# Optimization experiments

Hardware: AMD Instinct MI355X
Metric: run time of the kernel (lower is better)

## Reference

```python
import jax, jax.numpy as jnp
import numpy as np

GRID_SPACING = 0.5  # tf.constant(0.5)


def _mlp(x, W1, b1, W2, b2, W3, b3):
    # tiny base_model: 3 -> H -> H -> 1, positive output (softplus head)
    h = jnp.tanh(x @ W1 + b1)
    h = jnp.tanh(h @ W2 + b2)
    return jax.nn.softplus(h @ W3 + b3)


def setup_inputs() -> dict:
    key = jax.random.key(0)
    ks = jax.random.split(key, 8)
    nx = ny = nz = 128
    N = nx * ny * nz
    Ns = (nx - 1) * (ny - 1) * (nz - 1)
    B, H = 32768, 128
    DATAX = jax.random.uniform(ks[0], (N, 3), dtype=jnp.float32)
    DATAF = jax.random.uniform(ks[1], (N, 1), dtype=jnp.float32)
    STAGX = jax.random.uniform(ks[2], (Ns, 3), dtype=jnp.float32)
    LAPLF = jax.random.uniform(ks[3], (nx - 2, ny - 2, nz - 2), dtype=jnp.float32)
    center_indices = jax.random.randint(ks[4], (B,), 0, N, dtype=jnp.int32)
    W1 = jax.random.normal(ks[5], (3, H), dtype=jnp.float32) * 0.5
    W2 = jax.random.normal(ks[6], (H, H), dtype=jnp.float32) * (1.0 / np.sqrt(H))
    W3 = jax.random.normal(ks[7], (H, 1), dtype=jnp.float32) * (1.0 / np.sqrt(H))
    return {
        'DATAX': DATAX, 'DATAF': DATAF, 'STAGX': STAGX, 'LAPLF': LAPLF,
        'loss_m_weight': jnp.full((1,), 0.5, dtype=jnp.float32),
        'W1': W1, 'b1': jnp.zeros((H,), jnp.float32),
        'W2': W2, 'b2': jnp.zeros((H,), jnp.float32),
        'W3': W3, 'b3': jnp.zeros((1,), jnp.float32),
        'center_indices': center_indices,
    }


def reference(DATAX, DATAF, STAGX, LAPLF, loss_m_weight,
              W1, b1, W2, b2, W3, b3, center_indices):
    nxm2, nym2, nzm2 = LAPLF.shape
    nx, ny, nz = nxm2 + 2, nym2 + 2, nzm2 + 2
    N = nx * ny * nz
    Ns = (nx - 1) * (ny - 1) * (nz - 1)
    ci = center_indices.astype(jnp.int32)

    # decode flat id (z-major: z*nx*ny + y*nx + x)
    i_z = ci // (nx * ny)
    rem = ci % (nx * ny)
    i_y = rem // nx
    i_x = rem % nx
    valid = ((i_x >= 1) & (i_x < nx - 1) & (i_y >= 1) & (i_y < ny - 1)
             & (i_z >= 1) & (i_z < nz - 1))

    # 8 original-grid corners: dx,dy,dz in {-1,1}, dz fastest (list-comp order)
    off = jnp.array([-1, 1], jnp.int32)
    dd = jnp.stack(jnp.meshgrid(off, off, off, indexing='ij'), -1).reshape(8, 3)
    ox = i_x[:, None] + dd[None, :, 0]
    oy = i_y[:, None] + dd[None, :, 1]
    oz = i_z[:, None] + dd[None, :, 2]
    flat_o = jnp.clip(oz * nx * ny + oy * nx + ox, 0, N - 1)  # [B,8]

    # 8 staggered-grid corners: dx,dy,dz in {-1,0}, flat = x*ny'*nz' + y*nz' + z
    offs = jnp.array([-1, 0], jnp.int32)
    ds = jnp.stack(jnp.meshgrid(offs, offs, offs, indexing='ij'), -1).reshape(8, 3)
    sx = i_x[:, None] + ds[None, :, 0]
    sy = i_y[:, None] + ds[None, :, 1]
    sz = i_z[:, None] + ds[None, :, 2]
    flat_s = jnp.clip(sx * (ny - 1) * (nz - 1) + sy * (nz - 1) + sz, 0, Ns - 1)

    fo = _mlp(DATAX[flat_o], W1, b1, W2, b2, W3, b3)[..., 0]  # [B,8]
    fs = _mlp(STAGX[flat_s], W1, b1, W2, b2, W3, b3)[..., 0]  # [B,8]

    # diagonals of the [2,2,2] cube: (000,111),(010,101),(001,110),(011,100)
    ia = jnp.array([0, 2, 1, 3])
    ib = jnp.array([7, 5, 6, 4])
    num = jnp.abs(fo[:, ia] + fo[:, ib] - fs[:, ia] - fs[:, ib])
    den = fo[:, ia] + fo[:, ib] + fs[:, ia] + fs[:, ib]
    delta = 3.0 * (GRID_SPACING ** 2)
    lap = jnp.sum(num / den, axis=1) / (3.0 * delta)  # [B]

    flat_l = jnp.clip((i_x - 1) * nym2 * nzm2 + (i_y - 1) * nzm2 + (i_z - 1),
                      0, nxm2 * nym2 * nzm2 - 1)
    dlap = LAPLF.reshape(-1)[flat_l] - lap
    m = valid.astype(dlap.dtype)
    loss_m = loss_m_weight[0] * (jnp.sum(jnp.square(dlap) * m)
                                 / jnp.maximum(jnp.sum(m), 1.0))

    pred = _mlp(DATAX[ci], W1, b1, W2, b2, W3, b3)[:, 0]
    loss_e = jnp.mean(jnp.abs(pred - DATAF[ci][:, 0]))
    return loss_e + loss_m
```

## Files before the change

### kernel.cpp

```cpp
#include <hip/hip_runtime.h>
#include <stdint.h>

#define NXC   128
#define NXY   16384
#define NTOT  2097152
#define NS    2048383
#define SXY   16129
#define SYC   127
#define LXY   15876
#define LTOT  2000376

#define SCALE 2.8853900817779268f

typedef __bf16 bf16x8 __attribute__((ext_vector_type(8)));
typedef float f32x4 __attribute__((ext_vector_type(4)));

typedef const __attribute__((address_space(1))) uint32_t* gas_t;
typedef __attribute__((address_space(3))) uint32_t* las_t;

__device__ __forceinline__ float rcp_hw(float x) {
#if __has_builtin(__builtin_amdgcn_rcpf)
  return __builtin_amdgcn_rcpf(x);
#else
  return 1.0f / x;
#endif
}
__device__ __forceinline__ float exp2_hw(float x) {
#if __has_builtin(__builtin_amdgcn_exp2f)
  return __builtin_amdgcn_exp2f(x);
#else
  return __exp2f(x);
#endif
}

__device__ __forceinline__ float tanh_pre(float z) {
  float e = exp2_hw(z);
  return fmaf(-2.0f, rcp_hw(e + 1.0f), 1.0f);
}

__device__ __forceinline__ float softplus_f(float x) {
  float a = fabsf(x);
  return fmaxf(x, 0.0f) + __logf(1.0f + __expf(-a));
}

__device__ __forceinline__ void ld8(const float* p, float* o) {
  float4 a = *reinterpret_cast<const float4*>(p);
  float4 b = *reinterpret_cast<const float4*>(p + 4);
  o[0] = a.x; o[1] = a.y; o[2] = a.z; o[3] = a.w;
  o[4] = b.x; o[5] = b.y; o[6] = b.z; o[7] = b.w;
}

__global__ __launch_bounds__(256) void conv_kernel(
    const float* __restrict__ W1, const float* __restrict__ B1,
    const float* __restrict__ W2, const float* __restrict__ B2,
    const float* __restrict__ W3,
    __bf16* __restrict__ w2pre, float* __restrict__ smallpre)
{
  const int n = blockIdx.x * 256 + threadIdx.x;
  if (n < 2048) {
    const int c = n >> 7, j = n & 127;
    bf16x8 v;
    #pragma unroll
    for (int e = 0; e < 8; ++e) v[e] = (__bf16)(SCALE * W2[(8 * c + e) * 128 + j]);
    *reinterpret_cast<bf16x8*>(&w2pre[(j << 7) + (((c ^ (j & 15)) & 15) << 3)]) = v;
  }
  if (blockIdx.x == 0) {
    for (int i = threadIdx.x; i < 768; i += 256) {
      float v;
      if (i < 384)      v = SCALE * W1[i];
      else if (i < 512) v = SCALE * B1[i - 384];
      else if (i < 640) v = SCALE * B2[i - 512];
      else              v = W3[i - 640];
      smallpre[i] = v;
    }
  }
}

__global__ __launch_bounds__(512) void mlp_kernel(
    const float* __restrict__ DATAX, const float* __restrict__ STAGX,
    const int* __restrict__ CI,
    const __bf16* __restrict__ w2pre, const float* __restrict__ smallpre,
    const float* __restrict__ B3, float* __restrict__ fout)
{
  __shared__ __align__(16) __bf16 w2t[16384];
  __shared__ __align__(16) float smallb[768];

  const int tid  = threadIdx.x;
  const int lane = tid & 63;
  const int wid  = tid >> 6;
  const int cl   = lane & 15;
  const int g    = lane >> 4;

  const int group = (blockIdx.x << 3) + wid;
  const int gbase = group << 6;
  const int p = gbase + lane;
  const unsigned bb = (unsigned)p / 17u;
  const int t = p - (int)bb * 17;
  const int ci = CI[bb];

  {
    const char* gsrc = (const char*)w2pre + (wid << 12) + (lane << 4);
    char*       ldst = (char*)w2t + (wid << 12);
    #pragma unroll
    for (int i = 0; i < 4; ++i) {
      __builtin_amdgcn_global_load_lds(
          (gas_t)(const void*)(gsrc + (i << 10)),
          (las_t)(void*)(ldst + (i << 10)), 16, 0, 0);
    }
    if (wid == 7) {
      const char* gs = (const char*)smallpre + (lane << 4);
      char*       ld = (char*)smallb;
      #pragma unroll
      for (int i = 0; i < 3; ++i) {
        __builtin_amdgcn_global_load_lds(
            (gas_t)(const void*)(gs + (i << 10)),
            (las_t)(void*)(ld + (i << 10)), 16, 0, 0);
      }
    }
  }

  const int iz = ci >> 14, rem = ci & 16383, iy = rem >> 7, ix = rem & 127;
  const float* xp;
  if (t < 8) {
    int ox = ix + ((t & 4) ? 1 : -1);
    int oy = iy + ((t & 2) ? 1 : -1);
    int oz = iz + ((t & 1) ? 1 : -1);
    int fl = oz * NXY + oy * NXC + ox;
    fl = min(max(fl, 0), NTOT - 1);
    xp = DATAX + 3 * fl;
  } else if (t < 16) {
    int ts = t - 8;
    int sx = ix + ((ts & 4) ? 0 : -1);
    int sy = iy + ((ts & 2) ? 0 : -1);
    int sz = iz + ((ts & 1) ? 0 : -1);
    int fl = sx * SXY + sy * SYC + sz;
    fl = min(max(fl, 0), NS - 1);
    xp = STAGX + 3 * fl;
  } else {
    xp = DATAX + 3 * ci;
  }
  const float px = xp[0], py = xp[1], pz = xp[2];
  const float b3v = B3[0];

  __syncthreads();

  const float* w1s = smallb;
  const float* b1s = smallb + 384;
  const float* b2s = smallb + 512;
  const float* w3s = smallb + 640;

  float rxv[4], ryv[4], rzv[4];
  #pragma unroll
  for (int mt = 0; mt < 4; ++mt) {
    int src = (mt << 4) + cl;
    rxv[mt] = __shfl(px, src);
    ryv[mt] = __shfl(py, src);
    rzv[mt] = __shfl(pz, src);
  }

  bf16x8 A[4][4];
  #pragma unroll
  for (int kt = 0; kt < 4; ++kt) {
    int k0 = (kt << 5) + (g << 3);
    float wx[8], wy[8], wz[8], bv[8];
    ld8(&w1s[k0], wx);
    ld8(&w1s[128 + k0], wy);
    ld8(&w1s[256 + k0], wz);
    ld8(&b1s[k0], bv);
    #pragma unroll
    for (int mt = 0; mt < 4; ++mt) {
      #pragma unroll
      for (int e = 0; e < 8; ++e) {
        float pre = fmaf(rxv[mt], wx[e],
                    fmaf(ryv[mt], wy[e],
                    fmaf(rzv[mt], wz[e], bv[e])));
        A[mt][kt][e] = (__bf16)tanh_pre(pre);
      }
    }
  }

  float s[4][4];
  #pragma unroll
  for (int mt = 0; mt < 4; ++mt)
    #pragma unroll
    for (int r = 0; r < 4; ++r) s[mt][r] = 0.f;

  #pragma unroll
  for (int nt = 0; nt < 8; ++nt) {
    const float b2v = b2s[cl + (nt << 4)];
    const float w3v = w3s[cl + (nt << 4)];
    f32x4 cc[4];
    #pragma unroll
    for (int mt = 0; mt < 4; ++mt) {
      f32x4 seed = {b2v, b2v, b2v, b2v};
      cc[mt] = seed;
    }
    const int row = (nt << 4) + cl;
    #pragma unroll
    for (int kt = 0; kt < 4; ++kt) {
      int chunk = (kt << 2) + g;
      bf16x8 bfv = *reinterpret_cast<const bf16x8*>(
          &w2t[(row << 7) + ((chunk ^ cl) << 3)]);
      #pragma unroll
      for (int mt = 0; mt < 4; ++mt)
        cc[mt] = __builtin_amdgcn_mfma_f32_16x16x32_bf16(A[mt][kt], bfv, cc[mt], 0, 0, 0);
    }
    #pragma unroll
    for (int mt = 0; mt < 4; ++mt) {
      #pragma unroll
      for (int r = 0; r < 4; ++r) {
        float h2 = tanh_pre(cc[mt][r]);
        s[mt][r] = fmaf(h2, w3v, s[mt][r]);
      }
    }
  }

  #pragma unroll
  for (int mt = 0; mt < 4; ++mt) {
    #pragma unroll
    for (int r = 0; r < 4; ++r) {
      float v = s[mt][r];
      v += __shfl_xor(v, 1);
      v += __shfl_xor(v, 2);
      v += __shfl_xor(v, 4);
      v += __shfl_xor(v, 8);
      s[mt][r] = v;
    }
  }
  if (cl == 0) {
    #pragma unroll
    for (int mt = 0; mt < 4; ++mt) {
      int base = gbase + (mt << 4) + (g << 2);
      float4 o;
      o.x = softplus_f(s[mt][0] + b3v);
      o.y = softplus_f(s[mt][1] + b3v);
      o.z = softplus_f(s[mt][2] + b3v);
      o.w = softplus_f(s[mt][3] + b3v);
      *reinterpret_cast<float4*>(&fout[base]) = o;
    }
  }
}

__global__ __launch_bounds__(256) void reduce1(
    const float* __restrict__ f, const int* __restrict__ CI,
    const float* __restrict__ LAPLF, const float* __restrict__ DATAF,
    float* __restrict__ partials, int B)
{
  const int tid = threadIdx.x;
  const int b = blockIdx.x * 256 + tid;
  float sq = 0.f, mv = 0.f, ae = 0.f;
  if (b < B) {
    int ci = CI[b];
    int iz = ci >> 14, rem = ci & 16383, iy = rem >> 7, ix = rem & 127;
    bool valid = (ix >= 1) & (ix < 127) & (iy >= 1) & (iy < 127) &
                 (iz >= 1) & (iz < 127);
    const float* fb = f + b * 17;
    float fo[8], fs[8];
    #pragma unroll
    for (int i = 0; i < 8; ++i) { fo[i] = fb[i]; fs[i] = fb[8 + i]; }
    float pred = fb[16];
    const int ia[4] = {0, 2, 1, 3};
    const int ib[4] = {7, 5, 6, 4};
    float lap = 0.f;
    #pragma unroll
    for (int r = 0; r < 4; ++r) {
      float aa = fo[ia[r]] + fo[ib[r]];
      float bs = fs[ia[r]] + fs[ib[r]];
      lap += fabsf(aa - bs) / (aa + bs);
    }
    lap *= (1.0f / 2.25f);
    int fl = (ix - 1) * LXY + (iy - 1) * 126 + (iz - 1);
    fl = min(max(fl, 0), LTOT - 1);
    float dlap = LAPLF[fl] - lap;
    if (valid) { sq = dlap * dlap; mv = 1.f; }
    ae = fabsf(pred - DATAF[ci]);
  }
  #pragma unroll
  for (int msk = 32; msk >= 1; msk >>= 1) {
    sq += __shfl_xor(sq, msk);
    mv += __shfl_xor(mv, msk);
    ae += __shfl_xor(ae, msk);
  }
  __shared__ float rs[3][4];
  int lane = tid & 63, wd = tid >> 6;
  if (lane == 0) { rs[0][wd] = sq; rs[1][wd] = mv; rs[2][wd] = ae; }
  __syncthreads();
  if (tid == 0) {
    partials[blockIdx.x * 3 + 0] = rs[0][0] + rs[0][1] + rs[0][2] + rs[0][3];
    partials[blockIdx.x * 3 + 1] = rs[1][0] + rs[1][1] + rs[1][2] + rs[1][3];
    partials[blockIdx.x * 3 + 2] = rs[2][0] + rs[2][1] + rs[2][2] + rs[2][3];
  }
}

__global__ __launch_bounds__(128) void reduce2(
    const float* __restrict__ partials, const float* __restrict__ lw,
    float* __restrict__ out, int np, float invB)
{
  const int t = threadIdx.x;
  float sq = 0.f, mv = 0.f, ae = 0.f;
  for (int i = t; i < np; i += 128) {
    sq += partials[3 * i + 0];
    mv += partials[3 * i + 1];
    ae += partials[3 * i + 2];
  }
  #pragma unroll
  for (int msk = 32; msk >= 1; msk >>= 1) {
    sq += __shfl_xor(sq, msk);
    mv += __shfl_xor(mv, msk);
    ae += __shfl_xor(ae, msk);
  }
  __shared__ float rs[3][2];
  int lane = t & 63, wd = t >> 6;
  if (lane == 0) { rs[0][wd] = sq; rs[1][wd] = mv; rs[2][wd] = ae; }
  __syncthreads();
  if (t == 0) {
    float S = rs[0][0] + rs[0][1];
    float M = rs[1][0] + rs[1][1];
    float A = rs[2][0] + rs[2][1];
    out[0] = lw[0] * (S / fmaxf(M, 1.0f)) + A * invB;
  }
}

extern "C" void kernel_launch(void* const* d_in, const int* in_sizes, int n_in,
                              void* d_out, int out_size, void* d_ws, size_t ws_size,
                              hipStream_t stream) {
  const float* DATAX = (const float*)d_in[0];
  const float* DATAF = (const float*)d_in[1];
  const float* STAGX = (const float*)d_in[2];
  const float* LAPLF = (const float*)d_in[3];
  const float* LW    = (const float*)d_in[4];
  const float* W1    = (const float*)d_in[5];
  const float* B1    = (const float*)d_in[6];
  const float* W2    = (const float*)d_in[7];
  const float* B2    = (const float*)d_in[8];
  const float* W3    = (const float*)d_in[9];
  const float* B3    = (const float*)d_in[10];
  const int*   CI    = (const int*)d_in[11];

  const int B = in_sizes[11];
  const int P = 17 * B;
  const int ngroups = P >> 6;
  const int nblocks = ngroups >> 3;

  __bf16* w2pre    = (__bf16*)d_ws;
  float*  smallpre = (float*)((char*)d_ws + 32768);
  float*  fbuf     = (float*)((char*)d_ws + 36864);
  float*  partials = fbuf + P;

  conv_kernel<<<8, 256, 0, stream>>>(W1, B1, W2, B2, W3, w2pre, smallpre);
  mlp_kernel<<<nblocks, 512, 0, stream>>>(DATAX, STAGX, CI, w2pre, smallpre,
                                          B3, fbuf);
  const int nb2 = (B + 255) >> 8;
  reduce1<<<nb2, 256, 0, stream>>>(fbuf, CI, LAPLF, DATAF, partials, B);
  reduce2<<<1, 128, 0, stream>>>(partials, LW, (float*)d_out, nb2, 1.0f / (float)B);
}
```

Before: 68.59 us.

## Read MLP weights directly from global/L1 instead of staging in LDS

Removes the per-block async copy of the bf16 W2 matrix and small weight vectors into shared memory, along with the block barrier. The MFMA B-operands and bias/W3 values are now loaded straight from global memory and rely on cache hits. The bias and W3 vectors are interleaved so one float2 load fetches both. Blocks shrink from 512 to 256 threads, and the conversion kernel writes an unswizzled transposed W2 using more blocks. This drops the LDS fill and sync cost per block but puts repeated weight reads on the L1/L2 path, which may be slower than LDS.

```diff
diff --git a/kernel.cpp b/kernel.cpp
--- a/kernel.cpp
+++ b/kernel.cpp
@@ -15,9 +15,6 @@
 typedef __bf16 bf16x8 __attribute__((ext_vector_type(8)));
 typedef float f32x4 __attribute__((ext_vector_type(4)));
 
-typedef const __attribute__((address_space(1))) uint32_t* gas_t;
-typedef __attribute__((address_space(3))) uint32_t* las_t;
-
 __device__ __forceinline__ float rcp_hw(float x) {
 #if __has_builtin(__builtin_amdgcn_rcpf)
   return __builtin_amdgcn_rcpf(x);
@@ -57,67 +54,40 @@
     __bf16* __restrict__ w2pre, float* __restrict__ smallpre)
 {
   const int n = blockIdx.x * 256 + threadIdx.x;
-  if (n < 2048) {
-    const int c = n >> 7, j = n & 127;
-    bf16x8 v;
-    #pragma unroll
-    for (int e = 0; e < 8; ++e) v[e] = (__bf16)(SCALE * W2[(8 * c + e) * 128 + j]);
-    *reinterpret_cast<bf16x8*>(&w2pre[(j << 7) + (((c ^ (j & 15)) & 15) << 3)]) = v;
-  }
-  if (blockIdx.x == 0) {
-    for (int i = threadIdx.x; i < 768; i += 256) {
-      float v;
-      if (i < 384)      v = SCALE * W1[i];
-      else if (i < 512) v = SCALE * B1[i - 384];
-      else if (i < 640) v = SCALE * B2[i - 512];
-      else              v = W3[i - 640];
-      smallpre[i] = v;
-    }
-  }
-}
-
-__global__ __launch_bounds__(512) void mlp_kernel(
+  if (n < 16384) {
+    const int j = n >> 7, k = n & 127;
+    w2pre[n] = (__bf16)(SCALE * W2[k * 128 + j]);
+  }
+  if (n < 768) {
+    float v;
+    if (n < 384)      v = SCALE * W1[n];
+    else if (n < 512) v = SCALE * B1[n - 384];
+    else {
+      int q = (n - 512) >> 1;
+      v = ((n & 1) == 0) ? (SCALE * B2[q]) : W3[q];
+    }
+    smallpre[n] = v;
+  }
+}
+
+__global__ __launch_bounds__(256) void mlp_kernel(
     const float* __restrict__ DATAX, const float* __restrict__ STAGX,
     const int* __restrict__ CI,
     const __bf16* __restrict__ w2pre, const float* __restrict__ smallpre,
     const float* __restrict__ B3, float* __restrict__ fout)
 {
-  __shared__ __align__(16) __bf16 w2t[16384];
-  __shared__ __align__(16) float smallb[768];
-
   const int tid  = threadIdx.x;
   const int lane = tid & 63;
   const int wid  = tid >> 6;
   const int cl   = lane & 15;
   const int g    = lane >> 4;
 
-  const int group = (blockIdx.x << 3) + wid;
+  const int group = (blockIdx.x << 2) + wid;
   const int gbase = group << 6;
   const int p = gbase + lane;
   const unsigned bb = (unsigned)p / 17u;
   const int t = p - (int)bb * 17;
   const int ci = CI[bb];
-
-  {
-    const char* gsrc = (const char*)w2pre + (wid << 12) + (lane << 4);
-    char*       ldst = (char*)w2t + (wid << 12);
-    #pragma unroll
-    for (int i = 0; i < 4; ++i) {
-      __builtin_amdgcn_global_load_lds(
-          (gas_t)(const void*)(gsrc + (i << 10)),
-          (las_t)(void*)(ldst + (i << 10)), 16, 0, 0);
-    }
-    if (wid == 7) {
-      const char* gs = (const char*)smallpre + (lane << 4);
-      char*       ld = (char*)smallb;
-      #pragma unroll
-      for (int i = 0; i < 3; ++i) {
-        __builtin_amdgcn_global_load_lds(
-            (gas_t)(const void*)(gs + (i << 10)),
-            (las_t)(void*)(ld + (i << 10)), 16, 0, 0);
-      }
-    }
-  }
 
   const int iz = ci >> 14, rem = ci & 16383, iy = rem >> 7, ix = rem & 127;
   const float* xp;
@@ -142,13 +112,6 @@
   const float px = xp[0], py = xp[1], pz = xp[2];
   const float b3v = B3[0];
 
-  __syncthreads();
-
-  const float* w1s = smallb;
-  const float* b1s = smallb + 384;
-  const float* b2s = smallb + 512;
-  const float* w3s = smallb + 640;
-
   float rxv[4], ryv[4], rzv[4];
   #pragma unroll
   for (int mt = 0; mt < 4; ++mt) {
@@ -157,6 +120,10 @@
     ryv[mt] = __shfl(py, src);
     rzv[mt] = __shfl(pz, src);
   }
+
+  const float* w1s = smallpre;
+  const float* b1s = smallpre + 384;
+  const float* bw  = smallpre + 512;
 
   bf16x8 A[4][4];
   #pragma unroll
@@ -187,8 +154,8 @@
 
   #pragma unroll
   for (int nt = 0; nt < 8; ++nt) {
-    const float b2v = b2s[cl + (nt << 4)];
-    const float w3v = w3s[cl + (nt << 4)];
+    const float2 bwv = *reinterpret_cast<const float2*>(&bw[(cl + (nt << 4)) << 1]);
+    const float b2v = bwv.x, w3v = bwv.y;
     f32x4 cc[4];
     #pragma unroll
     for (int mt = 0; mt < 4; ++mt) {
@@ -198,9 +165,9 @@
     const int row = (nt << 4) + cl;
     #pragma unroll
     for (int kt = 0; kt < 4; ++kt) {
-      int chunk = (kt << 2) + g;
+      const int chunk = (kt << 2) + g;
       bf16x8 bfv = *reinterpret_cast<const bf16x8*>(
-          &w2t[(row << 7) + ((chunk ^ cl) << 3)]);
+          &w2pre[(row << 7) + (chunk << 3)]);
       #pragma unroll
       for (int mt = 0; mt < 4; ++mt)
         cc[mt] = __builtin_amdgcn_mfma_f32_16x16x32_bf16(A[mt][kt], bfv, cc[mt], 0, 0, 0);
@@ -340,15 +307,15 @@
   const int B = in_sizes[11];
   const int P = 17 * B;
   const int ngroups = P >> 6;
-  const int nblocks = ngroups >> 3;
+  const int nblocks = ngroups >> 2;
 
   __bf16* w2pre    = (__bf16*)d_ws;
   float*  smallpre = (float*)((char*)d_ws + 32768);
   float*  fbuf     = (float*)((char*)d_ws + 36864);
   float*  partials = fbuf + P;
 
-  conv_kernel<<<8, 256, 0, stream>>>(W1, B1, W2, B2, W3, w2pre, smallpre);
-  mlp_kernel<<<nblocks, 512, 0, stream>>>(DATAX, STAGX, CI, w2pre, smallpre,
+  conv_kernel<<<64, 256, 0, stream>>>(W1, B1, W2, B2, W3, w2pre, smallpre);
+  mlp_kernel<<<nblocks, 256, 0, stream>>>(DATAX, STAGX, CI, w2pre, smallpre,
                                           B3, fbuf);
   const int nb2 = (B + 255) >> 8;
   reduce1<<<nb2, 256, 0, stream>>>(fbuf, CI, LAPLF, DATAF, partials, B);
```

Result: slower. 74.65 us (+8.8%).
